# Kernel tuning notes

Measured on AMD Instinct MI355X. Metric: run time of the kernel, lower is better.

## Reference

```python
import jax, jax.numpy as jnp
import numpy as np


def log_g(x):
    # log of g(x) = relu(x)+0.5 for x>=0, sigmoid(x) for x<0 (continuous minGRU activation)
    return jnp.where(x >= 0, jnp.log(jax.nn.relu(x) + 0.5), -jax.nn.softplus(-x))


def parallel_scan_log(log_coeffs, log_values):
    # log_coeffs: [B,T,H], log_values: [B,T+1,H]
    a_star = jnp.pad(jnp.cumsum(log_coeffs, axis=1), ((0, 0), (1, 0), (0, 0)))  # [B,T+1,H]
    log_h = a_star + jax.lax.cumlogsumexp(log_values - a_star, axis=1)
    return jnp.exp(log_h)  # [B,T+1,H]


def setup_inputs() -> dict:
    key = jax.random.key(0)
    B, T, D, H = 8, 4096, 1024, 1024
    k1, k2, k3, k4, k5, k6 = jax.random.split(key, 6)
    scale = 1.0 / np.sqrt(D)
    return {
        "x": jax.random.normal(k1, (B, T, D), dtype=jnp.float32),
        "h_0": jax.random.uniform(k2, (B, 1, H), dtype=jnp.float32),
        "W_z": jax.random.uniform(k3, (H, D), minval=-scale, maxval=scale, dtype=jnp.float32),
        "b_z": jax.random.uniform(k4, (H,), minval=-scale, maxval=scale, dtype=jnp.float32),
        "W_h": jax.random.uniform(k5, (H, D), minval=-scale, maxval=scale, dtype=jnp.float32),
        "b_h": jax.random.uniform(k6, (H,), minval=-scale, maxval=scale, dtype=jnp.float32),
    }


def reference(x, h_0, W_z, b_z, W_h, b_h):
    # k = linear_z(x)
    k = jnp.einsum('btd,hd->bth', x, W_z) + b_z                 # [B,T,H]
    log_z = -jax.nn.softplus(-k)                                # log sigmoid(k)
    log_coeffs = -jax.nn.softplus(k)                            # log (1 - sigmoid(k))
    log_h_0 = log_g(h_0)                                        # [B,1,H]
    log_tilde_h = log_g(jnp.einsum('btd,hd->bth', x, W_h) + b_h)  # [B,T,H]
    log_values = jnp.concatenate([log_h_0, log_z + log_tilde_h], axis=1)  # [B,T+1,H]
    h = parallel_scan_log(log_coeffs, log_values)               # [B,T+1,H]
    return h
```

## Files before the change

kernel.cpp:

```cpp
#include <hip/hip_runtime.h>
#include <stdint.h>

#define B_ 8
#define T_ 4096
#define D_ 1024
#define H_ 1024
#define M_ (B_*T_)
#define K_ D_
#define N_ H_
#define TC 32
#define NC (T_/TC)

typedef short short8 __attribute__((ext_vector_type(8)));
typedef float f32x4 __attribute__((ext_vector_type(4)));
typedef unsigned short ushort8v __attribute__((ext_vector_type(8)));

__device__ __forceinline__ float bf2f(unsigned short u) {
    union { unsigned int i; float f; } x; x.i = ((unsigned int)u) << 16; return x.f;
}
__device__ __forceinline__ unsigned short f2bf(float f) {
    union { float f; unsigned int i; } x; x.f = f;
    unsigned int u = x.i;
    unsigned int r = u + 0x7fffu + ((u >> 16) & 1u);
    return (unsigned short)(r >> 16);
}
__device__ __forceinline__ void gld_lds16(const unsigned short* g, unsigned short* l) {
    __builtin_amdgcn_global_load_lds(
        (const __attribute__((address_space(1))) void*)(const void*)g,
        (__attribute__((address_space(3))) void*)(void*)l, 16, 0, 0);
}
__device__ __forceinline__ float sigm_neg(float k) {
    return __builtin_amdgcn_rcpf(1.f + __expf(k));
}
__device__ __forceinline__ float gfun(float x) {
    float neg = __builtin_amdgcn_rcpf(1.f + __expf(-x));
    return x >= 0.f ? x + 0.5f : neg;
}

__global__ void cvt_kernel(const float* __restrict__ src, unsigned short* __restrict__ dst, int n4) {
    int i = blockIdx.x * blockDim.x + threadIdx.x;
    const int stride = gridDim.x * blockDim.x;
    for (; i < n4; i += stride) {
        float4 v = ((const float4*)src)[i];
        ushort4 o;
        o.x = f2bf(v.x); o.y = f2bf(v.y); o.z = f2bf(v.z); o.w = f2bf(v.w);
        ((ushort4*)dst)[i] = o;
    }
}

__global__ void cvtw_kernel(const float* __restrict__ Wz, const float* __restrict__ Wh,
                            unsigned short* __restrict__ wzb, unsigned short* __restrict__ whb, int n4) {
    const float* src = blockIdx.y ? Wh : Wz;
    unsigned short* dst = blockIdx.y ? whb : wzb;
    int i = blockIdx.x * blockDim.x + threadIdx.x;
    const int stride = gridDim.x * blockDim.x;
    for (; i < n4; i += stride) {
        float4 v = ((const float4*)src)[i];
        ushort4 o;
        o.x = f2bf(v.x); o.y = f2bf(v.y); o.z = f2bf(v.z); o.w = f2bf(v.w);
        ((ushort4*)dst)[i] = o;
    }
}

#define SB() __builtin_amdgcn_sched_barrier(0)
#define BAR() do { SB(); __builtin_amdgcn_s_barrier(); SB(); } while (0)

__global__ __launch_bounds__(512, 2) void gemm_kernel(
    const unsigned short* __restrict__ Xb,
    const unsigned short* __restrict__ Wzb,
    const unsigned short* __restrict__ Whb,
    const float* __restrict__ bz, const float* __restrict__ bh,
    unsigned short* __restrict__ KzOut, unsigned short* __restrict__ KhOut,
    int row_off)
{
    __shared__ __align__(16) unsigned short ldsA[2][256 * 64];
    __shared__ __align__(16) unsigned short ldsB[2][256 * 64];

    const int bx = blockIdx.x;
    const int bn = blockIdx.y;
    const int mat = blockIdx.z;
    const unsigned short* Wb = mat ? Whb : Wzb;
    const float* bias = mat ? bh : bz;
    unsigned short* Out = mat ? KhOut : KzOut;

    const int tid = threadIdx.x;
    const int w = tid >> 6, lane = tid & 63;
    const int wm = w >> 2, wn = w & 3;

    const int srow = lane >> 3;
    const int schunk = ((lane & 7) ^ srow) << 3;
    const unsigned short* gA = Xb + (size_t)(row_off + bx * 512 + srow) * K_ + schunk;
    const unsigned short* gB = Wb + (size_t)(bn * 256 + srow) * K_ + schunk;

#define STAGE_A(s, g, h) do { \
    gld_lds16(gA + (size_t)(((g) >> 4) * 256 + (h)*128 + w*8) * K_ + ((g)&15) * 64, \
              &ldsA[s][((h)*128 + w*8) * 64]); \
    gld_lds16(gA + (size_t)(((g) >> 4) * 256 + (h)*128 + 64 + w*8) * K_ + ((g)&15) * 64, \
              &ldsA[s][((h)*128 + 64 + w*8) * 64]); \
  } while (0)
#define STAGE_B(s, g, h) do { \
    gld_lds16(gB + (size_t)((h)*128 + w*8) * K_ + ((g)&15) * 64, \
              &ldsB[s][((h)*128 + w*8) * 64]); \
    gld_lds16(gB + (size_t)((h)*128 + 64 + w*8) * K_ + ((g)&15) * 64, \
              &ldsB[s][((h)*128 + 64 + w*8) * 64]); \
  } while (0)

    const int lrow = lane & 15;
    const int q = lane >> 4;
    const int sw0 = (q ^ (lane & 7)) << 3;

#define LDA(s, fm, kh) (*(const short8*)&ldsA[s][(wm*128 + (fm)*16 + lrow) * 64 + (sw0 ^ ((kh)*32))])
#define LDB(s, fn, kh) (*(const short8*)&ldsB[s][(wn*64  + (fn)*16 + lrow) * 64 + (sw0 ^ ((kh)*32))])

#define RD_A4(s, fmb) do { \
    _Pragma("unroll") for (int f = 0; f < 4; ++f) { Ar[f][0] = LDA(s, (fmb)+f, 0); Ar[f][1] = LDA(s, (fmb)+f, 1); } \
  } while (0)
#define RD_B2(s, fnb) do { \
    _Pragma("unroll") for (int g2_ = 0; g2_ < 2; ++g2_) { Br[(fnb)+g2_][0] = LDB(s, (fnb)+g2_, 0); Br[(fnb)+g2_][1] = LDB(s, (fnb)+g2_, 1); } \
  } while (0)

#define QUAD(mb, nb) do { \
    __builtin_amdgcn_s_setprio(1); \
    _Pragma("unroll") for (int f = 0; f < 4; ++f) { \
      _Pragma("unroll") for (int g2_ = 0; g2_ < 2; ++g2_) { \
        acc[(mb)+f][(nb)+g2_] = __builtin_amdgcn_mfma_f32_16x16x32_bf16(Ar[f][0], Br[(nb)+g2_][0], acc[(mb)+f][(nb)+g2_], 0, 0, 0); \
        acc[(mb)+f][(nb)+g2_] = __builtin_amdgcn_mfma_f32_16x16x32_bf16(Ar[f][1], Br[(nb)+g2_][1], acc[(mb)+f][(nb)+g2_], 0, 0, 0); \
      } \
    } \
    __builtin_amdgcn_s_setprio(0); \
  } while (0)

    f32x4 acc[8][4];
    short8 Ar[4][2], Br[4][2];

    float bb[4];
#pragma unroll
    for (int fn = 0; fn < 4; ++fn) bb[fn] = bias[bn * 256 + wn * 64 + fn * 16 + lrow];

    STAGE_B(0, 0, 0); STAGE_B(0, 0, 1);
    STAGE_A(0, 0, 0); STAGE_A(0, 0, 1);
    STAGE_B(1, 1, 0); STAGE_B(1, 1, 1);
    SB();
    asm volatile("s_waitcnt vmcnt(4)" ::: "memory");
    BAR();

#pragma unroll 1
    for (int t = 0; t < 2; ++t) {
#pragma unroll
        for (int i = 0; i < 8; ++i)
#pragma unroll
            for (int j = 0; j < 4; ++j) acc[i][j] = (f32x4){0.f, 0.f, 0.f, 0.f};

#pragma unroll 1
        for (int i = 0; i < 8; ++i) {
            const int g1 = t * 16 + 2 * i + 1;
            const int g2 = g1 + 1;
            const int g3 = g1 + 2;
            const bool st = (g2 < 32);

            RD_A4(0, 0); RD_B2(0, 0);
            STAGE_A(1, g1, 0);
            BAR();
            QUAD(0, 0);
            BAR();
            RD_B2(0, 2);
            STAGE_A(1, g1, 1);
            BAR();
            QUAD(0, 2);
            BAR();
            RD_A4(0, 4);
            if (st) STAGE_B(0, g2, 0);
            BAR();
            QUAD(4, 0);
            BAR();
            if (st) {
                STAGE_B(0, g2, 1);
                SB();
                asm volatile("s_waitcnt vmcnt(4)" ::: "memory");
            } else {
                asm volatile("s_waitcnt vmcnt(0)" ::: "memory");
            }
            BAR();
            QUAD(4, 2);
            BAR();
            RD_A4(1, 0); RD_B2(1, 0);
            if (st) STAGE_A(0, g2, 0);
            BAR();
            QUAD(0, 0);
            BAR();
            RD_B2(1, 2);
            if (st) STAGE_A(0, g2, 1);
            BAR();
            QUAD(0, 2);
            BAR();
            RD_A4(1, 4);
            if (st) STAGE_B(1, g3, 0);
            BAR();
            QUAD(4, 0);
            BAR();
            if (st) {
                STAGE_B(1, g3, 1);
                SB();
                asm volatile("s_waitcnt vmcnt(4)" ::: "memory");
            }
            BAR();
            QUAD(4, 2);
            BAR();
        }

#pragma unroll
        for (int fn = 0; fn < 4; ++fn) {
            const int n = bn * 256 + wn * 64 + fn * 16 + lrow;
#pragma unroll
            for (int fm = 0; fm < 8; ++fm) {
                const int mq = (row_off >> 2) + bx * 128 + t * 64 + wm * 32 + fm * 4 + q;
                ushort4 o;
                o.x = f2bf(acc[fm][fn][0] + bb[fn]);
                o.y = f2bf(acc[fm][fn][1] + bb[fn]);
                o.z = f2bf(acc[fm][fn][2] + bb[fn]);
                o.w = f2bf(acc[fm][fn][3] + bb[fn]);
                *(ushort4*)(Out + ((size_t)mq * N_ + n) * 4) = o;
            }
        }
    }
}


#define QUAD_MATH(Z0, Z1, HH0, HH1, CYSTMT)                                            \
    _Pragma("unroll")                                                                  \
    for (int r = 0; r < 4; r++) {                                                      \
        float kzf[4] = {bf2f(Z0[r]), bf2f(Z0[4 + r]), bf2f(Z1[r]), bf2f(Z1[4 + r])};   \
        float khf[4] = {bf2f(HH0[r]), bf2f(HH0[4 + r]), bf2f(HH1[r]), bf2f(HH1[4 + r])};\
        _Pragma("unroll")                                                              \
        for (int j = 0; j < 4; j++) {                                                  \
            float f = sigm_neg(kzf[j]);                           \
            float v = (1.f - f) * gfun(khf[j]);                 \
            CYSTMT                                                                     \
        }                                                                              \
    }

__global__ __launch_bounds__(256) void scanA_kernel(const unsigned short* __restrict__ Kz,
                                                    const unsigned short* __restrict__ Kh,
                                                    float* __restrict__ Fc, float* __restrict__ Vc)
{
    const int c = blockIdx.x, b = blockIdx.y;
    const int hb = threadIdx.x * 4;
    float F[4] = {1.f, 1.f, 1.f, 1.f}, V[4] = {0.f, 0.f, 0.f, 0.f};
    const size_t base0 = ((size_t)(b * (T_ / 4) + c * (TC / 4)) * N_ + hb) * 4;
    const size_t str = (size_t)N_ * 4;
    ushort8v cz0 = *(const ushort8v*)(Kz + base0);
    ushort8v cz1 = *(const ushort8v*)(Kz + base0 + 8);
    ushort8v ch0 = *(const ushort8v*)(Kh + base0);
    ushort8v ch1 = *(const ushort8v*)(Kh + base0 + 8);
    ushort8v az0 = *(const ushort8v*)(Kz + base0 + str);
    ushort8v az1 = *(const ushort8v*)(Kz + base0 + str + 8);
    ushort8v ah0 = *(const ushort8v*)(Kh + base0 + str);
    ushort8v ah1 = *(const ushort8v*)(Kh + base0 + str + 8);
#pragma unroll 1
    for (int qq = 0; qq < TC / 4; qq++) {
        const int qn = (qq + 2 < TC / 4) ? qq + 2 : TC / 4 - 1;
        const size_t nb = base0 + (size_t)qn * str;
        ushort8v bz0 = *(const ushort8v*)(Kz + nb);
        ushort8v bz1 = *(const ushort8v*)(Kz + nb + 8);
        ushort8v bh0 = *(const ushort8v*)(Kh + nb);
        ushort8v bh1 = *(const ushort8v*)(Kh + nb + 8);
        QUAD_MATH(cz0, cz1, ch0, ch1, { V[j] = f * V[j] + v; F[j] *= f; })
        cz0 = az0; cz1 = az1; ch0 = ah0; ch1 = ah1;
        az0 = bz0; az1 = bz1; ah0 = bh0; ah1 = bh1;
    }
    size_t o = ((size_t)(b * NC + c)) * H_ + hb;
    *(float4*)(Fc + o) = make_float4(F[0], F[1], F[2], F[3]);
    *(float4*)(Vc + o) = make_float4(V[0], V[1], V[2], V[3]);
}

__global__ __launch_bounds__(64) void scanB_kernel(const float* __restrict__ h0,
                                                   const float* __restrict__ Fc,
                                                   const float* __restrict__ Vc,
                                                   float* __restrict__ Carry,
                                                   float* __restrict__ Out)
{
    const int b = blockIdx.x;
    const int h = blockIdx.y * 256 + threadIdx.x * 4;
    float cy[4];
#pragma unroll
    for (int j = 0; j < 4; j++) cy[j] = gfun(h0[(size_t)b * H_ + h + j]);
    *(float4*)(Out + (size_t)b * (T_ + 1) * H_ + h) = make_float4(cy[0], cy[1], cy[2], cy[3]);
    size_t o = ((size_t)(b * NC)) * H_ + h;
    float4 F4 = *(const float4*)(Fc + o);
    float4 V4 = *(const float4*)(Vc + o);
    for (int c = 0; c < NC; c++) {
        const size_t on = o + H_;
        float4 nF, nV;
        if (c + 1 < NC) {
            nF = *(const float4*)(Fc + on);
            nV = *(const float4*)(Vc + on);
        }
        *(float4*)(Carry + o) = make_float4(cy[0], cy[1], cy[2], cy[3]);
        cy[0] = F4.x * cy[0] + V4.x;
        cy[1] = F4.y * cy[1] + V4.y;
        cy[2] = F4.z * cy[2] + V4.z;
        cy[3] = F4.w * cy[3] + V4.w;
        F4 = nF; V4 = nV; o = on;
    }
}

__global__ __launch_bounds__(256) void scanC_kernel(const unsigned short* __restrict__ Kz,
                                                    const unsigned short* __restrict__ Kh,
                                                    const float* __restrict__ Carry,
                                                    float* __restrict__ Out)
{
    const int c = blockIdx.x, b = blockIdx.y;
    const int hb = threadIdx.x * 4;
    float cy[4];
    {
        float4 c4 = *(const float4*)(Carry + ((size_t)(b * NC + c)) * H_ + hb);
        cy[0] = c4.x; cy[1] = c4.y; cy[2] = c4.z; cy[3] = c4.w;
    }
    const size_t base0 = ((size_t)(b * (T_ / 4) + c * (TC / 4)) * N_ + hb) * 4;
    const size_t str = (size_t)N_ * 4;
    size_t ob = ((size_t)(b * (T_ + 1) + c * TC + 1)) * H_ + hb;
    ushort8v cz0 = *(const ushort8v*)(Kz + base0);
    ushort8v cz1 = *(const ushort8v*)(Kz + base0 + 8);
    ushort8v ch0 = *(const ushort8v*)(Kh + base0);
    ushort8v ch1 = *(const ushort8v*)(Kh + base0 + 8);
    ushort8v az0 = *(const ushort8v*)(Kz + base0 + str);
    ushort8v az1 = *(const ushort8v*)(Kz + base0 + str + 8);
    ushort8v ah0 = *(const ushort8v*)(Kh + base0 + str);
    ushort8v ah1 = *(const ushort8v*)(Kh + base0 + str + 8);
#pragma unroll 1
    for (int qq = 0; qq < TC / 4; qq++) {
        const int qn = (qq + 2 < TC / 4) ? qq + 2 : TC / 4 - 1;
        const size_t nb = base0 + (size_t)qn * str;
        ushort8v bz0 = *(const ushort8v*)(Kz + nb);
        ushort8v bz1 = *(const ushort8v*)(Kz + nb + 8);
        ushort8v bh0 = *(const ushort8v*)(Kh + nb);
        ushort8v bh1 = *(const ushort8v*)(Kh + nb + 8);
        QUAD_MATH(cz0, cz1, ch0, ch1, {
            cy[j] = f * cy[j] + v;
            if (j == 3) { *(float4*)(Out + ob) = make_float4(cy[0], cy[1], cy[2], cy[3]); ob += H_; }
        })
        cz0 = az0; cz1 = az1; ch0 = ah0; ch1 = ah1;
        az0 = bz0; az1 = bz1; ah0 = bh0; ah1 = bh1;
    }
}

extern "C" void kernel_launch(void* const* d_in, const int* in_sizes, int n_in,
                              void* d_out, int out_size, void* d_ws, size_t ws_size,
                              hipStream_t stream)
{
    const float* x  = (const float*)d_in[0];
    const float* h0 = (const float*)d_in[1];
    const float* Wz = (const float*)d_in[2];
    const float* bz = (const float*)d_in[3];
    const float* Wh = (const float*)d_in[4];
    const float* bh = (const float*)d_in[5];
    float* out = (float*)d_out;

    char* ws = (char*)d_ws;
    unsigned short* xb  = (unsigned short*)ws; ws += (size_t)M_ * K_ * 2;
    unsigned short* wzb = (unsigned short*)ws; ws += (size_t)N_ * K_ * 2;
    unsigned short* whb = (unsigned short*)ws; ws += (size_t)N_ * K_ * 2;
    unsigned short* kz  = (unsigned short*)ws; ws += (size_t)M_ * N_ * 2;
    unsigned short* kh  = (unsigned short*)ws; ws += (size_t)M_ * N_ * 2;
    float* Fc    = (float*)ws; ws += (size_t)B_ * NC * H_ * 4;
    float* Vc    = (float*)ws; ws += (size_t)B_ * NC * H_ * 4;
    float* Carry = (float*)ws; ws += (size_t)B_ * NC * H_ * 4;

    cvt_kernel<<<2048, 256, 0, stream>>>(x, xb, M_ * K_ / 4);
    cvtw_kernel<<<dim3(128, 2), 256, 0, stream>>>(Wz, Wh, wzb, whb, N_ * K_ / 4);

    dim3 gg(32, 4, 2);
    gemm_kernel<<<gg, 512, 0, stream>>>(xb, wzb, whb, bz, bh, kz, kh, 0);
    gemm_kernel<<<gg, 512, 0, stream>>>(xb, wzb, whb, bz, bh, kz, kh, 16384);

    scanA_kernel<<<dim3(NC, B_), 256, 0, stream>>>(kz, kh, Fc, Vc);
    scanB_kernel<<<dim3(B_, H_ / 256), 64, 0, stream>>>(h0, Fc, Vc, Carry, out);
    scanC_kernel<<<dim3(NC, B_), 256, 0, stream>>>(kz, kh, Carry, out);
}
```

Measured before the change: 450.1 us.

## Merge conversion and GEMM launches, fold carry scan into final scan kernel

```diff
diff --git a/kernel.cpp b/kernel.cpp
--- a/kernel.cpp
+++ b/kernel.cpp
@@ -37,7 +37,16 @@
     return x >= 0.f ? x + 0.5f : neg;
 }
 
-__global__ void cvt_kernel(const float* __restrict__ src, unsigned short* __restrict__ dst, int n4) {
+__global__ void cvt_all(const float* __restrict__ x, const float* __restrict__ Wz,
+                        const float* __restrict__ Wh,
+                        unsigned short* __restrict__ xb, unsigned short* __restrict__ wzb,
+                        unsigned short* __restrict__ whb) {
+    const float* src;
+    unsigned short* dst;
+    int n4;
+    if (blockIdx.y == 0)      { src = x;  dst = xb;  n4 = M_ * K_ / 4; }
+    else if (blockIdx.y == 1) { src = Wz; dst = wzb; n4 = N_ * K_ / 4; }
+    else                      { src = Wh; dst = whb; n4 = N_ * K_ / 4; }
     int i = blockIdx.x * blockDim.x + threadIdx.x;
     const int stride = gridDim.x * blockDim.x;
     for (; i < n4; i += stride) {
@@ -48,20 +57,6 @@
     }
 }
 
-__global__ void cvtw_kernel(const float* __restrict__ Wz, const float* __restrict__ Wh,
-                            unsigned short* __restrict__ wzb, unsigned short* __restrict__ whb, int n4) {
-    const float* src = blockIdx.y ? Wh : Wz;
-    unsigned short* dst = blockIdx.y ? whb : wzb;
-    int i = blockIdx.x * blockDim.x + threadIdx.x;
-    const int stride = gridDim.x * blockDim.x;
-    for (; i < n4; i += stride) {
-        float4 v = ((const float4*)src)[i];
-        ushort4 o;
-        o.x = f2bf(v.x); o.y = f2bf(v.y); o.z = f2bf(v.z); o.w = f2bf(v.w);
-        ((ushort4*)dst)[i] = o;
-    }
-}
-
 #define SB() __builtin_amdgcn_sched_barrier(0)
 #define BAR() do { SB(); __builtin_amdgcn_s_barrier(); SB(); } while (0)
 
@@ -70,8 +65,7 @@
     const unsigned short* __restrict__ Wzb,
     const unsigned short* __restrict__ Whb,
     const float* __restrict__ bz, const float* __restrict__ bh,
-    unsigned short* __restrict__ KzOut, unsigned short* __restrict__ KhOut,
-    int row_off)
+    unsigned short* __restrict__ KzOut, unsigned short* __restrict__ KhOut)
 {
     __shared__ __align__(16) unsigned short ldsA[2][256 * 64];
     __shared__ __align__(16) unsigned short ldsB[2][256 * 64];
@@ -89,7 +83,7 @@
 
     const int srow = lane >> 3;
     const int schunk = ((lane & 7) ^ srow) << 3;
-    const unsigned short* gA = Xb + (size_t)(row_off + bx * 512 + srow) * K_ + schunk;
+    const unsigned short* gA = Xb + (size_t)(bx * 1024 + srow) * K_ + schunk;
     const unsigned short* gB = Wb + (size_t)(bn * 256 + srow) * K_ + schunk;
 
 #define STAGE_A(s, g, h) do { \
@@ -145,7 +139,7 @@
     BAR();
 
 #pragma unroll 1
-    for (int t = 0; t < 2; ++t) {
+    for (int t = 0; t < 4; ++t) {
 #pragma unroll
         for (int i = 0; i < 8; ++i)
 #pragma unroll
@@ -156,7 +150,7 @@
             const int g1 = t * 16 + 2 * i + 1;
             const int g2 = g1 + 1;
             const int g3 = g1 + 2;
-            const bool st = (g2 < 32);
+            const bool st = (g2 < 64);
 
             RD_A4(0, 0); RD_B2(0, 0);
             STAGE_A(1, g1, 0);
@@ -213,7 +207,7 @@
             const int n = bn * 256 + wn * 64 + fn * 16 + lrow;
 #pragma unroll
             for (int fm = 0; fm < 8; ++fm) {
-                const int mq = (row_off >> 2) + bx * 128 + t * 64 + wm * 32 + fm * 4 + q;
+                const int mq = (bx * 4 + t) * 64 + wm * 32 + fm * 4 + q;
                 ushort4 o;
                 o.x = f2bf(acc[fm][fn][0] + bb[fn]);
                 o.y = f2bf(acc[fm][fn][1] + bb[fn]);
@@ -273,49 +267,50 @@
     *(float4*)(Vc + o) = make_float4(V[0], V[1], V[2], V[3]);
 }
 
-__global__ __launch_bounds__(64) void scanB_kernel(const float* __restrict__ h0,
-                                                   const float* __restrict__ Fc,
-                                                   const float* __restrict__ Vc,
-                                                   float* __restrict__ Carry,
-                                                   float* __restrict__ Out)
-{
-    const int b = blockIdx.x;
-    const int h = blockIdx.y * 256 + threadIdx.x * 4;
-    float cy[4];
-#pragma unroll
-    for (int j = 0; j < 4; j++) cy[j] = gfun(h0[(size_t)b * H_ + h + j]);
-    *(float4*)(Out + (size_t)b * (T_ + 1) * H_ + h) = make_float4(cy[0], cy[1], cy[2], cy[3]);
-    size_t o = ((size_t)(b * NC)) * H_ + h;
-    float4 F4 = *(const float4*)(Fc + o);
-    float4 V4 = *(const float4*)(Vc + o);
-    for (int c = 0; c < NC; c++) {
-        const size_t on = o + H_;
-        float4 nF, nV;
-        if (c + 1 < NC) {
-            nF = *(const float4*)(Fc + on);
-            nV = *(const float4*)(Vc + on);
-        }
-        *(float4*)(Carry + o) = make_float4(cy[0], cy[1], cy[2], cy[3]);
-        cy[0] = F4.x * cy[0] + V4.x;
-        cy[1] = F4.y * cy[1] + V4.y;
-        cy[2] = F4.z * cy[2] + V4.z;
-        cy[3] = F4.w * cy[3] + V4.w;
-        F4 = nF; V4 = nV; o = on;
-    }
-}
-
 __global__ __launch_bounds__(256) void scanC_kernel(const unsigned short* __restrict__ Kz,
                                                     const unsigned short* __restrict__ Kh,
-                                                    const float* __restrict__ Carry,
+                                                    const float* __restrict__ Fc,
+                                                    const float* __restrict__ Vc,
+                                                    const float* __restrict__ h0,
                                                     float* __restrict__ Out)
 {
     const int c = blockIdx.x, b = blockIdx.y;
     const int hb = threadIdx.x * 4;
+
     float cy[4];
+#pragma unroll
+    for (int k = 0; k < 4; ++k) cy[k] = gfun(h0[(size_t)b * H_ + hb + k]);
+    if (c == 0) {
+        *(float4*)(Out + (size_t)b * (T_ + 1) * H_ + hb) =
+            make_float4(cy[0], cy[1], cy[2], cy[3]);
+    }
     {
-        float4 c4 = *(const float4*)(Carry + ((size_t)(b * NC + c)) * H_ + hb);
-        cy[0] = c4.x; cy[1] = c4.y; cy[2] = c4.z; cy[3] = c4.w;
-    }
+        size_t o = ((size_t)(b * NC)) * H_ + hb;
+        int j = 0;
+        while (j < c) {
+            const int bnc = (c - j < 8) ? (c - j) : 8;
+            float4 Fb[8], Vb[8];
+#pragma unroll
+            for (int k = 0; k < 8; ++k) {
+                if (k < bnc) {
+                    Fb[k] = *(const float4*)(Fc + o + (size_t)k * H_);
+                    Vb[k] = *(const float4*)(Vc + o + (size_t)k * H_);
+                }
+            }
+#pragma unroll
+            for (int k = 0; k < 8; ++k) {
+                if (k < bnc) {
+                    cy[0] = Fb[k].x * cy[0] + Vb[k].x;
+                    cy[1] = Fb[k].y * cy[1] + Vb[k].y;
+                    cy[2] = Fb[k].z * cy[2] + Vb[k].z;
+                    cy[3] = Fb[k].w * cy[3] + Vb[k].w;
+                }
+            }
+            o += (size_t)bnc * H_;
+            j += bnc;
+        }
+    }
+
     const size_t base0 = ((size_t)(b * (T_ / 4) + c * (TC / 4)) * N_ + hb) * 4;
     const size_t str = (size_t)N_ * 4;
     size_t ob = ((size_t)(b * (T_ + 1) + c * TC + 1)) * H_ + hb;
@@ -364,16 +359,12 @@
     unsigned short* kh  = (unsigned short*)ws; ws += (size_t)M_ * N_ * 2;
     float* Fc    = (float*)ws; ws += (size_t)B_ * NC * H_ * 4;
     float* Vc    = (float*)ws; ws += (size_t)B_ * NC * H_ * 4;
-    float* Carry = (float*)ws; ws += (size_t)B_ * NC * H_ * 4;
-
-    cvt_kernel<<<2048, 256, 0, stream>>>(x, xb, M_ * K_ / 4);
-    cvtw_kernel<<<dim3(128, 2), 256, 0, stream>>>(Wz, Wh, wzb, whb, N_ * K_ / 4);
-
-    dim3 gg(32, 4, 2);
-    gemm_kernel<<<gg, 512, 0, stream>>>(xb, wzb, whb, bz, bh, kz, kh, 0);
-    gemm_kernel<<<gg, 512, 0, stream>>>(xb, wzb, whb, bz, bh, kz, kh, 16384);
+
+    cvt_all<<<dim3(2048, 3), 256, 0, stream>>>(x, Wz, Wh, xb, wzb, whb);
+
+    dim3 gg(M_ / 1024, N_ / 256, 2);
+    gemm_kernel<<<gg, 512, 0, stream>>>(xb, wzb, whb, bz, bh, kz, kh);
 
     scanA_kernel<<<dim3(NC, B_), 256, 0, stream>>>(kz, kh, Fc, Vc);
-    scanB_kernel<<<dim3(B_, H_ / 256), 64, 0, stream>>>(h0, Fc, Vc, Carry, out);
-    scanC_kernel<<<dim3(NC, B_), 256, 0, stream>>>(kz, kh, Carry, out);
-}
+    scanC_kernel<<<dim3(NC, B_), 256, 0, stream>>>(kz, kh, Fc, Vc, h0, out);
+}
```

New measurement: 442.1 us. About the same (-1.8%).
